# Optimization experiments

Measured on AMD Instinct MI355X. Metric: run time of the kernel, lower is better.

Reference implementation:

```python
import jax, jax.numpy as jnp
import numpy as np

VOCAB, D, H = 50257, 128, 128  # embedding_dim=128, lstm_size=128, num_layers=1
B, T = 64, 2048


def setup_inputs() -> dict:
    key = jax.random.key(0)
    ks = jax.random.split(key, 6)
    s = 1.0 / np.sqrt(H)  # PyTorch LSTM init scale
    return {
        "tokens": jax.random.randint(ks[0], (B, T), 0, VOCAB, dtype=jnp.int32),
        "emb_table": jax.random.normal(ks[1], (VOCAB, D), dtype=jnp.float32),
        "W_ih": jax.random.uniform(ks[2], (4 * H, D), jnp.float32, -s, s),
        "W_hh": jax.random.uniform(ks[3], (4 * H, H), jnp.float32, -s, s),
        "b_ih": jax.random.uniform(ks[4], (4 * H,), jnp.float32, -s, s),
        "b_hh": jax.random.uniform(ks[5], (4 * H,), jnp.float32, -s, s),
    }


def reference(tokens, emb_table, W_ih, W_hh, b_ih, b_hh):
    # Embedding lookup for the whole sequence: [B, T, D] -> time-major [T, B, D]
    x = jnp.swapaxes(emb_table[tokens], 0, 1)
    b = b_ih + b_hh  # fuse the two bias adds
    xg = jnp.einsum('tbd,gd->tbg', x, W_ih) + b  # precompute input gates [T, B, 4H]

    def step(carry, xt):
        h, c = carry
        gates = xt + h @ W_hh.T  # [B, 4H], PyTorch gate order i,f,g,o
        i, f, g, o = jnp.split(gates, 4, axis=-1)
        c2 = jax.nn.sigmoid(f) * c + jax.nn.sigmoid(i) * jnp.tanh(g)
        h2 = jax.nn.sigmoid(o) * jnp.tanh(c2)
        return (h2, c2), None

    h0 = jnp.zeros((tokens.shape[0], H), dtype=x.dtype)
    (h, c), _ = jax.lax.scan(step, (h0, h0), xg)
    # Original returns (state_h, state_c) each [num_layers=1, batch, H]
    return h[None], c[None]
```

## Files before the change

### kernel.cpp

```cpp
#include <hip/hip_runtime.h>
#include <hip/hip_bf16.h>


namespace {

constexpr int T_LEN  = 2048;
constexpr int Bsz    = 64;
constexpr int Dd     = 128;
constexpr int Hh     = 128;
constexpr int Gg     = 512;
constexpr int XS     = 136;
constexpr int NCHUNK = 256;
constexpr int CONS   = 64;
constexpr int PROD   = 192;
constexpr unsigned int SENT = 0x5EC7C0DEu;

typedef __attribute__((ext_vector_type(8))) short   short8;
typedef __attribute__((ext_vector_type(4))) float   floatx4;
typedef __attribute__((ext_vector_type(4))) int     intx4;
typedef __attribute__((ext_vector_type(2))) unsigned int uintx2;

#define MFMA16(a, b, c) __builtin_amdgcn_mfma_f32_16x16x32_bf16((a), (b), (c), 0, 0, 0)

#if __has_builtin(__builtin_amdgcn_sdot4)
__device__ __forceinline__ int dot4i8(int a, int b, int c) {
    return __builtin_amdgcn_sdot4(a, b, c, false);
}
#else
__device__ __forceinline__ int dot4i8(int a, int b, int c) {
#pragma unroll
    for (int j = 0; j < 4; ++j)
        c += ((a << (24 - 8 * j)) >> 24) * ((b << (24 - 8 * j)) >> 24);
    return c;
}
#endif

__device__ __forceinline__ int xor1_i(int v) {
    return __builtin_amdgcn_mov_dpp(v, 0xB1, 0xF, 0xF, true);
}

__device__ __forceinline__ float sigmoidf_(float x) {
    return __builtin_amdgcn_rcpf(1.0f + __builtin_amdgcn_exp2f(x * -1.44269504f));
}
__device__ __forceinline__ float tanhf_(float x) {
    return __builtin_fmaf(-2.0f,
        __builtin_amdgcn_rcpf(1.0f + __builtin_amdgcn_exp2f(x * 2.88539008f)), 1.0f);
}
__device__ __forceinline__ unsigned short f2bf(float f) {
    __hip_bfloat16 h = __float2bfloat16(f);
    union { __hip_bfloat16 b; unsigned short u; } v; v.b = h; return v.u;
}
__device__ __forceinline__ float fi_(unsigned int u) {
    union { unsigned int u; float f; } v; v.u = u; return v.f;
}
__device__ __forceinline__ int f_as_i(float f) {
    union { float f; int i; } v; v.f = f; return v.i;
}
__device__ __forceinline__ float i_as_f(int i) {
    union { int i; float f; } v; v.i = i; return v.f;
}
__device__ __forceinline__ uintx2 f4bf(const float4 v) {
    union { unsigned short us[4]; uintx2 u2; } p;
    p.us[0] = f2bf(v.x); p.us[1] = f2bf(v.y); p.us[2] = f2bf(v.z); p.us[3] = f2bf(v.w);
    return p.u2;
}
__device__ __forceinline__ short8 ld8bf(const float* p) {
    const float4 a = *reinterpret_cast<const float4*>(p);
    const float4 b = *reinterpret_cast<const float4*>(p + 4);
    short8 s;
    s[0] = (short)f2bf(a.x); s[1] = (short)f2bf(a.y);
    s[2] = (short)f2bf(a.z); s[3] = (short)f2bf(a.w);
    s[4] = (short)f2bf(b.x); s[5] = (short)f2bf(b.y);
    s[6] = (short)f2bf(b.z); s[7] = (short)f2bf(b.w);
    return s;
}
__device__ __forceinline__ void lds_barrier() {
    asm volatile("s_waitcnt lgkmcnt(0)\n\ts_barrier" ::: "memory");
}
__device__ __forceinline__ void wait_chunk(const unsigned int* flags, int k) {
    while (__hip_atomic_load(&flags[k], __ATOMIC_RELAXED,
                             __HIP_MEMORY_SCOPE_AGENT) != SENT)
        __builtin_amdgcn_s_sleep(2);
    __builtin_amdgcn_fence(__ATOMIC_ACQUIRE, "agent");
}
__device__ __forceinline__ void spin_chunk(const unsigned int* flags, int k) {
    while (__hip_atomic_load(&flags[k], __ATOMIC_RELAXED,
                             __HIP_MEMORY_SCOPE_AGENT) != SENT)
        __builtin_amdgcn_s_sleep(2);
}

__global__ __launch_bounds__(256) void lstm_fused_all(
    const int*   __restrict__ tokens,
    const float* __restrict__ emb,
    const float* __restrict__ Wih,
    const float* __restrict__ Whh,
    const float* __restrict__ bih,
    const float* __restrict__ bhh,
    unsigned short* __restrict__ xg,
    unsigned int*   __restrict__ flags,
    float*       __restrict__ out)
{
    __shared__ __align__(16) unsigned short albs[2][64 * XS];

    const int tid = threadIdx.x;

    if (blockIdx.x < CONS) {
        __builtin_amdgcn_s_setprio(1);
        signed char (*hbuf)[128] =
            reinterpret_cast<signed char (*)[128]>(&albs[0][0]);

        const int wv = tid >> 6;
        const int l  = tid & 63;
        const int gh = l & 1;
        const int c  = wv * 32 + (l >> 1);
        const int b  = blockIdx.x;

        const float kf = gh ? 1.0f : 2.0f;
        const float kb = gh ? 0.0f : -1.0f;
        const int   sh = gh ? 0 : 16;

        int   wq[2][32];
        float dq[2];
#pragma unroll
        for (int q = 0; q < 2; ++q) {
            const int g = q * 2 + gh;
            const float* wr = Whh + (size_t)(g * 128 + c) * Hh;
            float am = 0.f;
#pragma unroll 8
            for (int k = 0; k < 128; k += 4) {
                const float4 v = *reinterpret_cast<const float4*>(wr + k);
                am = fmaxf(am, fmaxf(fmaxf(fabsf(v.x), fabsf(v.y)),
                                     fmaxf(fabsf(v.z), fabsf(v.w))));
            }
            const float swm = fmaxf(am, 1e-20f);
            dq[q] = swm * (1.0f / (127.0f * 127.0f));
            const float inv = 127.0f / swm;
#pragma unroll
            for (int d = 0; d < 32; ++d) {
                const float4 v = *reinterpret_cast<const float4*>(wr + d * 4);
                const int b0 = (int)__builtin_rintf(v.x * inv);
                const int b1 = (int)__builtin_rintf(v.y * inv);
                const int b2 = (int)__builtin_rintf(v.z * inv);
                const int b3 = (int)__builtin_rintf(v.w * inv);
                wq[q][d] = (b0 & 0xff) | ((b1 & 0xff) << 8) |
                           ((b2 & 0xff) << 16) | ((b3 & 0xff) << 24);
            }
        }

        intx4 hv[8];
#pragma unroll
        for (int j = 0; j < 8; ++j) hv[j] = (intx4){0, 0, 0, 0};

        const unsigned short* xptr = xg + (size_t)b * Gg + c * 4;
        const size_t xstride = (size_t)Bsz * Gg;

        wait_chunk(flags, 0);
        uintx2 xc[8];
#pragma unroll
        for (int u = 0; u < 8; ++u)
            xc[u] = *reinterpret_cast<const uintx2*>(xptr + (size_t)u * xstride);
        wait_chunk(flags, 1);

        float c_state = 0.0f;
        float h_last  = 0.0f;
        unsigned int fpre = SENT;

        for (int g = 0; g < NCHUNK; ++g) {
            int tn = g + 1;
            if (tn >= NCHUNK) tn = 0;
            const size_t tb = (size_t)tn * 8;
#pragma unroll
            for (int s = 0; s < 8; ++s) {
                const uintx2 xv = xc[s];

                if (s >= 1)
                    xc[s - 1] = *reinterpret_cast<const uintx2*>(
                        xptr + (tb + (s - 1)) * xstride);
                if (s == 7)
                    xc[7] = *reinterpret_cast<const uintx2*>(
                        xptr + (tb + 7) * xstride);

                if (s == 2) {
                    if (g + 2 < NCHUNK)
                        fpre = __hip_atomic_load(&flags[g + 2], __ATOMIC_RELAXED,
                                                 __HIP_MEMORY_SCOPE_AGENT);
                }
                if (s == 4) {
                    if (g + 2 < NCHUNK && fpre != SENT) spin_chunk(flags, g + 2);
                }

                int b0 = 0, b1 = 0, b2 = 0, b3 = 0;
#pragma unroll
                for (int j = 0; j < 8; ++j) {
                    const intx4 h4 = hv[j];
                    b0 = dot4i8(wq[1][j * 4 + 0], h4[0], b0);
                    b1 = dot4i8(wq[1][j * 4 + 1], h4[1], b1);
                    b2 = dot4i8(wq[1][j * 4 + 2], h4[2], b2);
                    b3 = dot4i8(wq[1][j * 4 + 3], h4[3], b3);
                }
                const int m1 = (b0 + b1) + (b2 + b3);

                const float x1 = fi_((xv.y << sh) & 0xffff0000u);
                const float g1 = (float)m1 * dq[1] + x1;
                const float r2 = sigmoidf_(g1 * kf);
                const float v2 = __builtin_fmaf(r2, kf, kb);
                const float so127 = v2 * 127.0f;

                int a0 = 0, a1 = 0, a2 = 0, a3 = 0;
#pragma unroll
                for (int j = 0; j < 8; ++j) {
                    const intx4 h4 = hv[j];
                    a0 = dot4i8(wq[0][j * 4 + 0], h4[0], a0);
                    a1 = dot4i8(wq[0][j * 4 + 1], h4[1], a1);
                    a2 = dot4i8(wq[0][j * 4 + 2], h4[2], a2);
                    a3 = dot4i8(wq[0][j * 4 + 3], h4[3], a3);
                }
                const int m0 = (a0 + a1) + (a2 + a3);

                const float x0 = fi_((xv.x << sh) & 0xffff0000u);
                const float g0 = (float)m0 * dq[0] + x0;
                const float r1 = sigmoidf_(g0);
                const float A  = r1 * v2;
                const float swv = i_as_f(xor1_i(f_as_i(gh ? r1 : A)));
                const float F   = gh ? r1 : swv;
                const float Ag  = gh ? swv : A;
                c_state = __builtin_fmaf(F, c_state, Ag);
                const float t2 = tanhf_(c_state);
                h_last = v2 * t2;

                const int nxt = (s & 1) ^ 1;
                if (gh == 1) {
                    const int q =
                        f_as_i(__builtin_fmaf(so127, t2, 12582912.0f));
                    hbuf[nxt][c] = (signed char)(q & 0xff);
                }
                lds_barrier();
#pragma unroll
                for (int j = 0; j < 8; ++j)
                    hv[j] = *reinterpret_cast<const intx4*>(
                        &hbuf[nxt][j * 16]);
            }
        }

        if (gh == 1) {
            out[b * Hh + c]            = h_last;
            out[Bsz * Hh + b * Hh + c] = c_state;
        }
    } else {
        const int pid  = blockIdx.x - CONS;
        const int wv   = tid >> 6;
        const int l    = tid & 63;
        const int quad = l >> 4;
        const int cl   = l & 15;
        const int srow = tid >> 2, sseg = tid & 3;

        float bias[2][4];
#pragma unroll
        for (int jj = 0; jj < 2; ++jj) {
            const int hhj = (wv * 2 + jj) * 16 + cl;
#pragma unroll
            for (int g = 0; g < 4; ++g)
                bias[jj][g] = bih[g * 128 + hhj] + bhh[g * 128 + hhj];
        }

        for (int chunk = pid; chunk < NCHUNK; chunk += PROD) {
            const int t0 = chunk * 8;

            {
                const int tok = tokens[srow * T_LEN + t0];
                const float* src = emb + (size_t)tok * Dd + sseg * 32;
#pragma unroll
                for (int p = 0; p < 4; ++p)
                    *reinterpret_cast<short8*>(
                        &albs[0][srow * XS + sseg * 32 + p * 8]) = ld8bf(src + p * 8);
            }
            __syncthreads();

            for (int tt = 0; tt < 8; ++tt) {
                const int cur = tt & 1, nxt = cur ^ 1;
                if (tt < 7) {
                    const int tok = tokens[srow * T_LEN + t0 + tt + 1];
                    const float* src = emb + (size_t)tok * Dd + sseg * 32;
#pragma unroll
                    for (int p = 0; p < 4; ++p)
                        *reinterpret_cast<short8*>(
                            &albs[nxt][srow * XS + sseg * 32 + p * 8]) =
                            ld8bf(src + p * 8);
                }

                short8 af[4][4];
#pragma unroll
                for (int m = 0; m < 4; ++m)
#pragma unroll
                    for (int k = 0; k < 4; ++k)
                        af[m][k] = *reinterpret_cast<const short8*>(
                            &albs[cur][(m * 16 + cl) * XS + k * 32 + quad * 8]);

                const int t = t0 + tt;
#pragma unroll
                for (int jj = 0; jj < 2; ++jj) {
                    const int hhj = (wv * 2 + jj) * 16 + cl;
                    floatx4 acc[4][4];
#pragma unroll
                    for (int g = 0; g < 4; ++g)
#pragma unroll
                        for (int m = 0; m < 4; ++m)
                            acc[g][m] = (floatx4){0.f, 0.f, 0.f, 0.f};
#pragma unroll
                    for (int g = 0; g < 4; ++g) {
                        const int n = g * 128 + hhj;
                        short8 bf[4];
#pragma unroll
                        for (int k = 0; k < 4; ++k)
                            bf[k] = ld8bf(Wih + (size_t)n * Dd + k * 32 + quad * 8);
#pragma unroll
                        for (int k = 0; k < 4; ++k)
#pragma unroll
                            for (int m = 0; m < 4; ++m)
                                acc[g][m] = MFMA16(af[m][k], bf[k], acc[g][m]);
                    }
#pragma unroll
                    for (int m = 0; m < 4; ++m) {
#pragma unroll
                        for (int r = 0; r < 4; ++r) {
                            const int brow = m * 16 + quad * 4 + r;
                            union { unsigned short us[4]; uintx2 u2; } p;
#pragma unroll
                            for (int g = 0; g < 4; ++g)
                                p.us[g] = f2bf(acc[g][m][r] + bias[jj][g]);
                            *reinterpret_cast<uintx2*>(
                                xg + ((size_t)t * Bsz + brow) * Gg + hhj * 4) =
                                p.u2;
                        }
                    }
                }
                __syncthreads();
            }

            if (tid == 0) {
                __builtin_amdgcn_fence(__ATOMIC_RELEASE, "agent");
                __hip_atomic_store(&flags[chunk], SENT, __ATOMIC_RELAXED,
                                   __HIP_MEMORY_SCOPE_AGENT);
            }
        }
    }
}

__global__ __launch_bounds__(512, 2) void lstm_fused_fb(
    const int*   __restrict__ tokens,
    const float* __restrict__ emb,
    const float* __restrict__ Wih,
    const float* __restrict__ Whh,
    const float* __restrict__ bih,
    const float* __restrict__ bhh,
    float*       __restrict__ out)
{
    __shared__ unsigned short xbuf[2][16 * XS];
    __shared__ unsigned short hbuf2[2][16 * XS];
    __shared__ float scratch[4 * Gg];

    const int tid  = threadIdx.x;
    const int w    = tid >> 6;
    const int l    = tid & 63;
    const int quad = l >> 4;
    const int cl   = l & 15;
    const int bbase = blockIdx.x * 4;
    const int rr = tid >> 7;
    const int hh = tid & 127;

    short8 wih[4][4], whh[4][4];
    float  bias[4];
#pragma unroll
    for (int q = 0; q < 4; ++q) {
        const int n = q * 128 + w * 16 + cl;
#pragma unroll
        for (int kk = 0; kk < 4; ++kk) {
            const int k0 = kk * 32 + quad * 8;
            wih[q][kk] = ld8bf(Wih + n * Dd + k0);
            whh[q][kk] = ld8bf(Whh + n * Hh + k0);
        }
        bias[q] = bih[n] + bhh[n];
    }

    for (int i = tid; i < 16 * XS; i += 512) {
        xbuf[0][i] = 0; xbuf[1][i] = 0; hbuf2[0][i] = 0; hbuf2[1][i] = 0;
    }

    const bool gact = (tid < 128);
    const int  gr = tid >> 5;
    const int  gp = tid & 31;
    float4 gdataf = {0.f, 0.f, 0.f, 0.f};
    if (gact) {
        const int tok = tokens[(bbase + gr) * T_LEN + 0];
        gdataf = *reinterpret_cast<const float4*>(emb + (size_t)tok * Dd + gp * 4);
    }
    __syncthreads();
    if (gact) *reinterpret_cast<uintx2*>(&xbuf[0][gr * XS + gp * 4]) = f4bf(gdataf);
    if (gact) {
        const int tok = tokens[(bbase + gr) * T_LEN + 1];
        gdataf = *reinterpret_cast<const float4*>(emb + (size_t)tok * Dd + gp * 4);
    }
    __syncthreads();

    const int afrag_el = cl * XS + quad * 8;

    floatx4 acc[4];
#pragma unroll
    for (int q = 0; q < 4; ++q) acc[q] = (floatx4){bias[q], bias[q], bias[q], bias[q]};
    {
        short8 xf[4];
#pragma unroll
        for (int kk = 0; kk < 4; ++kk)
            xf[kk] = *reinterpret_cast<const short8*>(&xbuf[0][afrag_el + kk * 32]);
#pragma unroll
        for (int kk = 0; kk < 4; ++kk)
#pragma unroll
            for (int q = 0; q < 4; ++q)
                acc[q] = MFMA16(xf[kk], wih[q][kk], acc[q]);
    }

    float c_state = 0.0f, h_last = 0.0f;

    for (int t = 0; t < T_LEN; ++t) {
        const int cur = t & 1, nxt = cur ^ 1;
        short8 hf[4];
#pragma unroll
        for (int kk = 0; kk < 4; ++kk)
            hf[kk] = *reinterpret_cast<const short8*>(&hbuf2[cur][afrag_el + kk * 32]);
        if (gact && (t + 1 < T_LEN))
            *reinterpret_cast<uintx2*>(&xbuf[nxt][gr * XS + gp * 4]) = f4bf(gdataf);
        if (gact && (t + 2 < T_LEN)) {
            const int tok = tokens[(bbase + gr) * T_LEN + (t + 2)];
            gdataf = *reinterpret_cast<const float4*>(emb + (size_t)tok * Dd + gp * 4);
        }
#pragma unroll
        for (int kk = 0; kk < 4; ++kk)
#pragma unroll
            for (int q = 0; q < 4; ++q)
                acc[q] = MFMA16(hf[kk], whh[q][kk], acc[q]);
        if (quad == 0) {
#pragma unroll
            for (int q = 0; q < 4; ++q) {
                const int n = q * 128 + w * 16 + cl;
#pragma unroll
                for (int r = 0; r < 4; ++r)
                    scratch[r * Gg + n] = acc[q][r];
            }
        }
        __syncthreads();
#pragma unroll
        for (int q = 0; q < 4; ++q) acc[q] = (floatx4){bias[q], bias[q], bias[q], bias[q]};
        if (t + 1 < T_LEN) {
            short8 xf[4];
#pragma unroll
            for (int kk = 0; kk < 4; ++kk)
                xf[kk] = *reinterpret_cast<const short8*>(&xbuf[nxt][afrag_el + kk * 32]);
#pragma unroll
            for (int kk = 0; kk < 4; ++kk)
#pragma unroll
                for (int q = 0; q < 4; ++q)
                    acc[q] = MFMA16(xf[kk], wih[q][kk], acc[q]);
        }
        {
            const float iv = scratch[rr * Gg + hh];
            const float fv = scratch[rr * Gg + 128 + hh];
            const float gv = scratch[rr * Gg + 256 + hh];
            const float ov = scratch[rr * Gg + 384 + hh];
            const float si = sigmoidf_(iv);
            const float sf = sigmoidf_(fv);
            const float so = sigmoidf_(ov);
            const float tg = tanhf_(gv);
            c_state = sf * c_state + si * tg;
            h_last  = so * tanhf_(c_state);
            hbuf2[nxt][rr * XS + hh] = f2bf(h_last);
        }
        __syncthreads();
    }

    const int ob = (bbase + rr) * Hh + hh;
    out[ob]            = h_last;
    out[Bsz * Hh + ob] = c_state;
}

}

extern "C" void kernel_launch(void* const* d_in, const int* in_sizes, int n_in,
                              void* d_out, int out_size, void* d_ws, size_t ws_size,
                              hipStream_t stream) {
    (void)in_sizes; (void)n_in; (void)out_size;
    const int*   tokens = (const int*)d_in[0];
    const float* emb    = (const float*)d_in[1];
    const float* Wih    = (const float*)d_in[2];
    const float* Whh    = (const float*)d_in[3];
    const float* bih    = (const float*)d_in[4];
    const float* bhh    = (const float*)d_in[5];

    const size_t xg_bytes = (size_t)T_LEN * Bsz * Gg * sizeof(unsigned short);
    const size_t need = xg_bytes + NCHUNK * sizeof(unsigned int);
    if (ws_size >= need) {
        unsigned short* xg    = (unsigned short*)d_ws;
        unsigned int*   flags = (unsigned int*)((char*)d_ws + xg_bytes);
        lstm_fused_all<<<CONS + PROD, 256, 0, stream>>>(
            tokens, emb, Wih, Whh, bih, bhh, xg, flags, (float*)d_out);
    } else {
        lstm_fused_fb<<<16, 512, 0, stream>>>(tokens, emb, Wih, Whh, bih, bhh,
                                              (float*)d_out);
    }
}
```

Before: 820.9 us.

## Process two batch rows per consumer block and shift blocks to producers

Each recurrent consumer block now advances two batch sequences at once, sharing the register-resident int8 W_hh across both. This halves the consumer block count from 64 to 32, and the freed blocks become input-gate producers (192 to 224). Interleaving two independent recurrences is meant to hide the dot-product and transcendental latency of the serial chain behind each other, and to amortise the per-step LDS barrier over two rows. The cost is roughly double the per-step work on the critical path in each consumer, plus higher register pressure from the duplicated h vectors and prefetch buffers.

Result: slower. 1.375 ms (+67.5%).

```diff
diff --git a/kernel.cpp b/kernel.cpp
--- a/kernel.cpp
+++ b/kernel.cpp
@@ -11,8 +11,8 @@
 constexpr int Gg     = 512;
 constexpr int XS     = 136;
 constexpr int NCHUNK = 256;
-constexpr int CONS   = 64;
-constexpr int PROD   = 192;
+constexpr int CONS   = 32;
+constexpr int PROD   = 224;
 constexpr unsigned int SENT = 0x5EC7C0DEu;
 
 typedef __attribute__((ext_vector_type(8))) short   short8;
@@ -106,14 +106,15 @@
 
     if (blockIdx.x < CONS) {
         __builtin_amdgcn_s_setprio(1);
-        signed char (*hbuf)[128] =
-            reinterpret_cast<signed char (*)[128]>(&albs[0][0]);
+        signed char (*hbuf)[2][128] =
+            reinterpret_cast<signed char (*)[2][128]>(&albs[0][0]);
 
         const int wv = tid >> 6;
         const int l  = tid & 63;
         const int gh = l & 1;
         const int c  = wv * 32 + (l >> 1);
-        const int b  = blockIdx.x;
+        const int bA = blockIdx.x * 2;
+        const int bB = bA + 1;
 
         const float kf = gh ? 1.0f : 2.0f;
         const float kb = gh ? 0.0f : -1.0f;
@@ -147,22 +148,28 @@
             }
         }
 
-        intx4 hv[8];
-#pragma unroll
-        for (int j = 0; j < 8; ++j) hv[j] = (intx4){0, 0, 0, 0};
-
-        const unsigned short* xptr = xg + (size_t)b * Gg + c * 4;
+        intx4 hvA[8], hvB[8];
+#pragma unroll
+        for (int j = 0; j < 8; ++j) {
+            hvA[j] = (intx4){0, 0, 0, 0};
+            hvB[j] = (intx4){0, 0, 0, 0};
+        }
+
+        const unsigned short* xptrA = xg + (size_t)bA * Gg + c * 4;
+        const unsigned short* xptrB = xg + (size_t)bB * Gg + c * 4;
         const size_t xstride = (size_t)Bsz * Gg;
 
         wait_chunk(flags, 0);
-        uintx2 xc[8];
-#pragma unroll
-        for (int u = 0; u < 8; ++u)
-            xc[u] = *reinterpret_cast<const uintx2*>(xptr + (size_t)u * xstride);
+        uintx2 xcA[8], xcB[8];
+#pragma unroll
+        for (int u = 0; u < 8; ++u) {
+            xcA[u] = *reinterpret_cast<const uintx2*>(xptrA + (size_t)u * xstride);
+            xcB[u] = *reinterpret_cast<const uintx2*>(xptrB + (size_t)u * xstride);
+        }
         wait_chunk(flags, 1);
 
-        float c_state = 0.0f;
-        float h_last  = 0.0f;
+        float cA = 0.0f, hA = 0.0f;
+        float cB = 0.0f, hB = 0.0f;
         unsigned int fpre = SENT;
 
         for (int g = 0; g < NCHUNK; ++g) {
@@ -171,14 +178,21 @@
             const size_t tb = (size_t)tn * 8;
 #pragma unroll
             for (int s = 0; s < 8; ++s) {
-                const uintx2 xv = xc[s];
-
-                if (s >= 1)
-                    xc[s - 1] = *reinterpret_cast<const uintx2*>(
-                        xptr + (tb + (s - 1)) * xstride);
-                if (s == 7)
-                    xc[7] = *reinterpret_cast<const uintx2*>(
-                        xptr + (tb + 7) * xstride);
+                const uintx2 xvA = xcA[s];
+                const uintx2 xvB = xcB[s];
+
+                if (s >= 1) {
+                    xcA[s - 1] = *reinterpret_cast<const uintx2*>(
+                        xptrA + (tb + (s - 1)) * xstride);
+                    xcB[s - 1] = *reinterpret_cast<const uintx2*>(
+                        xptrB + (tb + (s - 1)) * xstride);
+                }
+                if (s == 7) {
+                    xcA[7] = *reinterpret_cast<const uintx2*>(
+                        xptrA + (tb + 7) * xstride);
+                    xcB[7] = *reinterpret_cast<const uintx2*>(
+                        xptrB + (tb + 7) * xstride);
+                }
 
                 if (s == 2) {
                     if (g + 2 < NCHUNK)
@@ -189,62 +203,116 @@
                     if (g + 2 < NCHUNK && fpre != SENT) spin_chunk(flags, g + 2);
                 }
 
-                int b0 = 0, b1 = 0, b2 = 0, b3 = 0;
+                int a1A0 = 0, a1A1 = 0, a1A2 = 0, a1A3 = 0;
 #pragma unroll
                 for (int j = 0; j < 8; ++j) {
-                    const intx4 h4 = hv[j];
-                    b0 = dot4i8(wq[1][j * 4 + 0], h4[0], b0);
-                    b1 = dot4i8(wq[1][j * 4 + 1], h4[1], b1);
-                    b2 = dot4i8(wq[1][j * 4 + 2], h4[2], b2);
-                    b3 = dot4i8(wq[1][j * 4 + 3], h4[3], b3);
-                }
-                const int m1 = (b0 + b1) + (b2 + b3);
-
-                const float x1 = fi_((xv.y << sh) & 0xffff0000u);
-                const float g1 = (float)m1 * dq[1] + x1;
-                const float r2 = sigmoidf_(g1 * kf);
-                const float v2 = __builtin_fmaf(r2, kf, kb);
-                const float so127 = v2 * 127.0f;
-
-                int a0 = 0, a1 = 0, a2 = 0, a3 = 0;
+                    const intx4 h4 = hvA[j];
+                    a1A0 = dot4i8(wq[1][j * 4 + 0], h4[0], a1A0);
+                    a1A1 = dot4i8(wq[1][j * 4 + 1], h4[1], a1A1);
+                    a1A2 = dot4i8(wq[1][j * 4 + 2], h4[2], a1A2);
+                    a1A3 = dot4i8(wq[1][j * 4 + 3], h4[3], a1A3);
+                }
+                const int m1A = (a1A0 + a1A1) + (a1A2 + a1A3);
+
+                int a1B0 = 0, a1B1 = 0, a1B2 = 0, a1B3 = 0;
 #pragma unroll
                 for (int j = 0; j < 8; ++j) {
-                    const intx4 h4 = hv[j];
-                    a0 = dot4i8(wq[0][j * 4 + 0], h4[0], a0);
-                    a1 = dot4i8(wq[0][j * 4 + 1], h4[1], a1);
-                    a2 = dot4i8(wq[0][j * 4 + 2], h4[2], a2);
-                    a3 = dot4i8(wq[0][j * 4 + 3], h4[3], a3);
-                }
-                const int m0 = (a0 + a1) + (a2 + a3);
-
-                const float x0 = fi_((xv.x << sh) & 0xffff0000u);
-                const float g0 = (float)m0 * dq[0] + x0;
-                const float r1 = sigmoidf_(g0);
-                const float A  = r1 * v2;
-                const float swv = i_as_f(xor1_i(f_as_i(gh ? r1 : A)));
-                const float F   = gh ? r1 : swv;
-                const float Ag  = gh ? swv : A;
-                c_state = __builtin_fmaf(F, c_state, Ag);
-                const float t2 = tanhf_(c_state);
-                h_last = v2 * t2;
+                    const intx4 h4 = hvB[j];
+                    a1B0 = dot4i8(wq[1][j * 4 + 0], h4[0], a1B0);
+                    a1B1 = dot4i8(wq[1][j * 4 + 1], h4[1], a1B1);
+                    a1B2 = dot4i8(wq[1][j * 4 + 2], h4[2], a1B2);
+                    a1B3 = dot4i8(wq[1][j * 4 + 3], h4[3], a1B3);
+                }
+                const int m1B = (a1B0 + a1B1) + (a1B2 + a1B3);
+
+                const float x1A = fi_((xvA.y << sh) & 0xffff0000u);
+                const float g1A = (float)m1A * dq[1] + x1A;
+                const float r2A = sigmoidf_(g1A * kf);
+                const float v2A = __builtin_fmaf(r2A, kf, kb);
+                const float so127A = v2A * 127.0f;
+
+                const float x1B = fi_((xvB.y << sh) & 0xffff0000u);
+                const float g1B = (float)m1B * dq[1] + x1B;
+                const float r2B = sigmoidf_(g1B * kf);
+                const float v2B = __builtin_fmaf(r2B, kf, kb);
+                const float so127B = v2B * 127.0f;
+
+                int a0A0 = 0, a0A1 = 0, a0A2 = 0, a0A3 = 0;
+#pragma unroll
+                for (int j = 0; j < 8; ++j) {
+                    const intx4 h4 = hvA[j];
+                    a0A0 = dot4i8(wq[0][j * 4 + 0], h4[0], a0A0);
+                    a0A1 = dot4i8(wq[0][j * 4 + 1], h4[1], a0A1);
+                    a0A2 = dot4i8(wq[0][j * 4 + 2], h4[2], a0A2);
+                    a0A3 = dot4i8(wq[0][j * 4 + 3], h4[3], a0A3);
+                }
+                const int m0A = (a0A0 + a0A1) + (a0A2 + a0A3);
+
+                int a0B0 = 0, a0B1 = 0, a0B2 = 0, a0B3 = 0;
+#pragma unroll
+                for (int j = 0; j < 8; ++j) {
+                    const intx4 h4 = hvB[j];
+                    a0B0 = dot4i8(wq[0][j * 4 + 0], h4[0], a0B0);
+                    a0B1 = dot4i8(wq[0][j * 4 + 1], h4[1], a0B1);
+                    a0B2 = dot4i8(wq[0][j * 4 + 2], h4[2], a0B2);
+                    a0B3 = dot4i8(wq[0][j * 4 + 3], h4[3], a0B3);
+                }
+                const int m0B = (a0B0 + a0B1) + (a0B2 + a0B3);
 
                 const int nxt = (s & 1) ^ 1;
-                if (gh == 1) {
-                    const int q =
-                        f_as_i(__builtin_fmaf(so127, t2, 12582912.0f));
-                    hbuf[nxt][c] = (signed char)(q & 0xff);
-                }
+
+                {
+                    const float x0 = fi_((xvA.x << sh) & 0xffff0000u);
+                    const float g0 = (float)m0A * dq[0] + x0;
+                    const float r1 = sigmoidf_(g0);
+                    const float Aa = r1 * v2A;
+                    const float swv = i_as_f(xor1_i(f_as_i(gh ? r1 : Aa)));
+                    const float F   = gh ? r1 : swv;
+                    const float Ag  = gh ? swv : Aa;
+                    cA = __builtin_fmaf(F, cA, Ag);
+                    const float t2 = tanhf_(cA);
+                    hA = v2A * t2;
+                    if (gh == 1) {
+                        const int q =
+                            f_as_i(__builtin_fmaf(so127A, t2, 12582912.0f));
+                        hbuf[0][nxt][c] = (signed char)(q & 0xff);
+                    }
+                }
+                {
+                    const float x0 = fi_((xvB.x << sh) & 0xffff0000u);
+                    const float g0 = (float)m0B * dq[0] + x0;
+                    const float r1 = sigmoidf_(g0);
+                    const float Ab = r1 * v2B;
+                    const float swv = i_as_f(xor1_i(f_as_i(gh ? r1 : Ab)));
+                    const float F   = gh ? r1 : swv;
+                    const float Ag  = gh ? swv : Ab;
+                    cB = __builtin_fmaf(F, cB, Ag);
+                    const float t2 = tanhf_(cB);
+                    hB = v2B * t2;
+                    if (gh == 1) {
+                        const int q =
+                            f_as_i(__builtin_fmaf(so127B, t2, 12582912.0f));
+                        hbuf[1][nxt][c] = (signed char)(q & 0xff);
+                    }
+                }
+
                 lds_barrier();
 #pragma unroll
                 for (int j = 0; j < 8; ++j)
-                    hv[j] = *reinterpret_cast<const intx4*>(
-                        &hbuf[nxt][j * 16]);
+                    hvA[j] = *reinterpret_cast<const intx4*>(
+                        &hbuf[0][nxt][j * 16]);
+#pragma unroll
+                for (int j = 0; j < 8; ++j)
+                    hvB[j] = *reinterpret_cast<const intx4*>(
+                        &hbuf[1][nxt][j * 16]);
             }
         }
 
         if (gh == 1) {
-            out[b * Hh + c]            = h_last;
-            out[Bsz * Hh + b * Hh + c] = c_state;
+            out[bA * Hh + c]            = hA;
+            out[Bsz * Hh + bA * Hh + c] = cA;
+            out[bB * Hh + c]            = hB;
+            out[Bsz * Hh + bB * Hh + c] = cB;
         }
     } else {
         const int pid  = blockIdx.x - CONS;
```
